# Performance work log

Measured on AMD Instinct MI355X. Metric: run time of the kernel, lower is better.

The kernel has to match this reference:

```python
import jax, jax.numpy as jnp
import numpy as np

ITER_STEPS = 2


def setup_inputs() -> dict:
    key = jax.random.key(0)
    ks = jax.random.split(key, 9)
    B, N, D, E = 64, 256, 512, 10  # batch, nodes, node_dim, edge types
    node = jax.random.normal(ks[0], (B, N, D), dtype=jnp.float32)
    node_mask = jax.random.randint(ks[1], (B, N), 0, 2).astype(jnp.int32)
    adj = jax.random.randint(ks[2], (E, B, N, N), 0, 2).astype(jnp.int32)
    s = 0.02
    W_nw = jax.random.normal(ks[3], (1, D), dtype=jnp.float32) * s   # node weight fc [out=1, in=D]
    b_nw = jnp.zeros((1,), dtype=jnp.float32)
    W_self = jax.random.normal(ks[4], (D, D), dtype=jnp.float32) * s
    b_self = jnp.zeros((D,), dtype=jnp.float32)
    W_edge = jax.random.normal(ks[5], (E, D, D), dtype=jnp.float32) * s  # per-edge-type Linear (no bias)
    return {"node": node, "W_nw": W_nw, "b_nw": b_nw, "W_self": W_self,
            "b_self": b_self, "W_edge": W_edge, "node_mask": node_mask, "adj": adj}


def reference(node, W_nw, b_nw, W_self, b_self, W_edge, node_mask, adj):
    # node: [B,N,D]; node_mask: [B,N] int; adj: [E=10,B,N,N] int (binary)
    B, N, D = node.shape
    m = node_mask.astype(node.dtype)
    eye = jnp.eye(N, dtype=node.dtype)
    # dd_graph = mask outer-product with zeroed diagonal: [B,N,N]
    dd = m[:, None, :] * m[:, :, None] * (1.0 - eye)
    graphs = dd[None] * adj.astype(node.dtype)  # [E,B,N,N]
    # total neighbor count across all 10 edge types, clamped to >=1 (replace_masked_values)
    neigh = graphs.sum(axis=(0, 3))                       # [B,N]
    neigh = jnp.where(neigh >= 1.0, neigh, 1.0)
    all_weight = []
    for _ in range(ITER_STEPS):
        # (1) node relatedness gate
        w = jax.nn.sigmoid(node @ W_nw.T + b_nw)[..., 0]  # [B,N]
        all_weight.append(w)
        self_info = node @ W_self.T + b_self              # [B,N,D]
        # (2) per-edge-type projection + masked adjacency matmul, summed over edge types
        proj = jnp.einsum('bnk,edk->ebnd', node, W_edge)  # [E,B,N,D]
        masked_w = jnp.where(graphs != 0, w[None, :, None, :], 0.0)  # [E,B,N,N]
        agg = jnp.einsum('ebnm,ebmd->bnd', masked_w, proj)           # [B,N,D]
        # (3) update
        node = jax.nn.relu(self_info + agg / neigh[..., None])
    return node, jnp.stack(all_weight, axis=1)  # ([B,N,D], [B,ITER,N])
```

## Files before the change

### kernel.cpp

```cpp
#include <hip/hip_runtime.h>
#include <hip/hip_bf16.h>

#define BB 64
#define NN 256
#define DD 512
#define EE 10

typedef __bf16 bf16x8 __attribute__((ext_vector_type(8)));
typedef unsigned short ushort8v __attribute__((ext_vector_type(8)));
typedef unsigned int uint4v __attribute__((ext_vector_type(4)));
typedef unsigned int uint2v __attribute__((ext_vector_type(2)));
typedef float floatx4 __attribute__((ext_vector_type(4)));
typedef float floatx16 __attribute__((ext_vector_type(16)));

typedef __attribute__((address_space(3))) unsigned short lds_us;
typedef const __attribute__((address_space(1))) unsigned short glb_us;

__device__ __forceinline__ unsigned short f2b(float f) {
    union { float f; unsigned u; } x; x.f = f;
    unsigned r = x.u + 0x7FFFu + ((x.u >> 16) & 1u);
    return (unsigned short)(r >> 16);
}
__device__ __forceinline__ float b2f(unsigned short u) {
    union { unsigned u; float f; } x; x.u = ((unsigned)u) << 16;
    return x.f;
}
__device__ __forceinline__ unsigned pack_bf16(float a, float b) {
    union { float f; unsigned u; } xa, xb2; xa.f = a; xb2.f = b;
    return __builtin_amdgcn_perm(xa.u + 0x8000u, xb2.u + 0x8000u, 0x07060302u);
}
__device__ __forceinline__ bf16x8 expand_byte(unsigned byte_) {
    uint4v av;
    #pragma unroll
    for (int p2 = 0; p2 < 4; p2++) {
        unsigned tt = (byte_ >> (2 * p2)) & 3u;
        av[p2] = ((tt | (tt << 15)) & 0x10001u) * 0x3F80u;
    }
    return __builtin_bit_cast(bf16x8, av);
}

__global__ void k_wconv(const float* __restrict__ W_edge,
                        const float* __restrict__ W_self,
                        unsigned short* __restrict__ Wf) {
    int t = blockIdx.x * 256 + threadIdx.x;
    int lane  = t & 63;
    int kstep = (t >> 6) & 31;
    int cfg   = (t >> 11) & 15;
    int e     = t >> 15;
    int dout = cfg * 32 + (lane & 31);
    int k    = kstep * 16 + (lane >> 5) * 8;
    const float* src = (e < EE) ? (W_edge + ((size_t)e * DD + dout) * DD + k)
                                : (W_self + (size_t)dout * DD + k);
    ushort8v o;
    #pragma unroll
    for (int j = 0; j < 8; j++) o[j] = f2b(src[j]);
    *(ushort8v*)(Wf + (size_t)t * 8) = o;
}

__global__ void k_graph(const int* __restrict__ adj, const int* __restrict__ mask,
                        unsigned* __restrict__ packed, float* __restrict__ recip) {
    int b = blockIdx.x >> 8;
    int n = blockIdx.x & 255;
    int lane = threadIdx.x & 63;
    int wv   = threadIdx.x >> 6;
    int m = wv * 64 + lane;
    int ok = (mask[b * NN + n] != 0) & (mask[b * NN + m] != 0) & (m != n);
    __shared__ int cnt_s[4];
    int total = 0;
    #pragma unroll
    for (int e = 0; e < EE; e++) {
        int a = adj[(((size_t)e * BB + b) * NN + n) * NN + m];
        int bit = ok & (a != 0);
        unsigned long long bal = __ballot(bit);
        if (lane == 0) {
            unsigned* dst = packed + (((size_t)e * BB + b) * NN + n) * 8 + wv * 2;
            dst[0] = (unsigned)bal;
            dst[1] = (unsigned)(bal >> 32);
        }
        total += bit;
    }
    for (int off = 32; off; off >>= 1) total += __shfl_down(total, off);
    if (lane == 0) cnt_s[wv] = total;
    __syncthreads();
    if (threadIdx.x == 0) {
        int c = cnt_s[0] + cnt_s[1] + cnt_s[2] + cnt_s[3];
        recip[b * NN + n] = 1.0f / (float)(c < 1 ? 1 : c);
    }
}

template<int TI>
__global__ __launch_bounds__(256)
void k_gt(const float* __restrict__ xf, const unsigned short* __restrict__ xbin,
          const float* __restrict__ W_nw, const float* __restrict__ b_nw,
          float* __restrict__ w_out, unsigned short* __restrict__ wTf,
          unsigned short* __restrict__ xb0) {
    int bid = blockIdx.x;
    int b  = bid >> 4;
    int ms = bid & 15;
    __shared__ float part[16][17];
    __shared__ float wsig[16];
    int t = threadIdx.x;
    int row = t >> 4;
    int seg = t & 15;
    size_t g = ((size_t)(b * NN + ms * 16 + row)) * DD + seg * 32;
    float s = 0.f;
    if (TI == 0) {
        const floatx4* xp = (const floatx4*)(xf + g);
        const floatx4* wp = (const floatx4*)(W_nw + seg * 32);
        #pragma unroll
        for (int k = 0; k < 4; k++) {
            floatx4 a = xp[2 * k], c4 = xp[2 * k + 1];
            floatx4 wa = wp[2 * k], wc = wp[2 * k + 1];
            ushort8v u;
            #pragma unroll
            for (int j = 0; j < 4; j++) {
                s += a[j] * wa[j] + c4[j] * wc[j];
                u[j] = f2b(a[j]); u[4 + j] = f2b(c4[j]);
            }
            *(ushort8v*)(xb0 + g + k * 8) = u;
        }
    } else {
        const ushort8v* xp = (const ushort8v*)(xbin + g);
        const float* wp = W_nw + seg * 32;
        #pragma unroll
        for (int k = 0; k < 4; k++) {
            ushort8v u = xp[k];
            #pragma unroll
            for (int j = 0; j < 8; j++) s += b2f(u[j]) * wp[k * 8 + j];
        }
    }
    part[row][seg] = s;
    __syncthreads();
    if (t < 16) {
        float tot = 0.f;
        #pragma unroll
        for (int i = 0; i < 16; i++) tot += part[t][i];
        float v = 1.f / (1.f + __expf(-(tot + b_nw[0])));
        wsig[t] = v;
        w_out[(b * 2 + TI) * NN + ms * 16 + t] = v;
    }
    __syncthreads();
    #pragma unroll
    for (int c = 0; c < 4; c++) {
        int slot = t + 256 * c;
        int dd_  = slot >> 6;
        int lane = slot & 63;
        int l31 = lane & 31, hi = lane >> 5;
        size_t xrow = ((size_t)(b * NN + ms * 16 + hi * 8)) * DD + dd_ * 32 + l31;
        ushort8v o;
        #pragma unroll
        for (int j = 0; j < 8; j++) {
            float xv = (TI == 0) ? xf[xrow + (size_t)j * DD] : b2f(xbin[xrow + (size_t)j * DD]);
            o[j] = f2b(xv * wsig[hi * 8 + j]);
        }
        *(ushort8v*)(wTf + ((((size_t)b * 16 + ms) * 16 + dd_) * 64 + lane) * 8) = o;
    }
}

template<int TI>
__global__ __launch_bounds__(512, 4)
void k2_heavy(const unsigned short* __restrict__ wTf,
              const unsigned short* __restrict__ xb,
              const unsigned short* __restrict__ Wf,
              const unsigned* __restrict__ packed,
              const float* __restrict__ recip,
              const float* __restrict__ b_self,
              unsigned short* __restrict__ out_bf16,
              float* __restrict__ out_f32) {
    __shared__ __attribute__((aligned(16))) unsigned short sWT[64 * 512];
    __shared__ __attribute__((aligned(16))) unsigned short sTf[16 * 512];

    int bid = blockIdx.x;
    int ct = bid & 1;
    int b  = (bid >> 1) & 63;
    int nq = bid >> 7;
    int w = threadIdx.x >> 6, lane = threadIdx.x & 63;
    int l31 = lane & 31, hi = lane >> 5;

    int s1_d = w >> 1, s1_nb = w & 1;
    int gn1 = nq * 64 + s1_nb * 32 + l31;
    float rn = recip[b * NN + gn1];

    floatx16 acc2[2];
    #pragma unroll
    for (int i = 0; i < 2; i++)
        #pragma unroll
        for (int q = 0; q < 16; q++) acc2[i][q] = 0.f;

    auto stage_sWT = [&](int dc2) {
        #pragma unroll
        for (int it = 0; it < 8; it++) {
            int c = it * 8 + w;
            const unsigned short* g = wTf +
                ((((size_t)b * 16 + (c >> 2)) * 16 + dc2 * 4 + (c & 3)) * 64 + lane) * 8;
            __builtin_amdgcn_global_load_lds((glb_us*)g, (lds_us*)&sWT[c * 512], 16, 0, 0);
        }
    };

    stage_sWT(0);

    const unsigned short* WfL = Wf + lane * 8;
    const unsigned short* xbL = xb + ((size_t)(b * NN + nq * 64 + l31)) * DD + hi * 8;

    unsigned pw[8];

    #pragma unroll 1
    for (int s = 0; s < 40; s++) {
        int e = s >> 2, dc2 = s & 3;
        asm volatile("s_waitcnt vmcnt(0) lgkmcnt(0)" ::: "memory");
        __builtin_amdgcn_s_barrier();
        if ((s & 3) == 0) {
            const uint4v* pp = (const uint4v*)(packed +
                (((size_t)e * BB + b) * NN + gn1) * 8);
            uint4v pa = pp[0], pbv = pp[1];
            pw[0] = pa[0]; pw[1] = pa[1]; pw[2] = pa[2]; pw[3] = pa[3];
            pw[4] = pbv[0]; pw[5] = pbv[1]; pw[6] = pbv[2]; pw[7] = pbv[3];
        }
        {
            floatx16 acc3a, acc3b;
            #pragma unroll
            for (int q = 0; q < 16; q++) { acc3a[q] = 0.f; acc3b[q] = 0.f; }
            #pragma unroll
            for (int ks = 0; ks < 8; ks++) {
                bf16x8 afrA = __builtin_bit_cast(bf16x8,
                    *(const ushort8v*)&sWT[((2 * ks) * 4 + s1_d) * 512 + lane * 8]);
                bf16x8 afrB = __builtin_bit_cast(bf16x8,
                    *(const ushort8v*)&sWT[((2 * ks + 1) * 4 + s1_d) * 512 + lane * 8]);
                unsigned wrd = pw[ks];
                bf16x8 bgA = expand_byte((wrd >> (hi * 8)) & 0xFFu);
                bf16x8 bgB = expand_byte((wrd >> ((2 + hi) * 8)) & 0xFFu);
                acc3a = __builtin_amdgcn_mfma_f32_32x32x16_bf16(afrA, bgA, acc3a, 0, 0, 0);
                acc3b = __builtin_amdgcn_mfma_f32_32x32x16_bf16(afrB, bgB, acc3b, 0, 0, 0);
            }
            #pragma unroll
            for (int g = 0; g < 4; g++) {
                float v0 = (acc3a[g * 4 + 0] + acc3b[g * 4 + 0]) * rn;
                float v1 = (acc3a[g * 4 + 1] + acc3b[g * 4 + 1]) * rn;
                float v2 = (acc3a[g * 4 + 2] + acc3b[g * 4 + 2]) * rn;
                float v3 = (acc3a[g * 4 + 3] + acc3b[g * 4 + 3]) * rn;
                uint2v pk;
                pk[0] = pack_bf16(v1, v0);
                pk[1] = pack_bf16(v3, v2);
                int kk_w = s1_d * 2 + (g >> 1);
                int slot = (kk_w * 2 + s1_nb) * 64 + (g & 1) * 32 + l31;
                *(uint2v*)&sTf[slot * 8 + 4 * hi] = pk;
            }
        }
        asm volatile("s_waitcnt lgkmcnt(0)" ::: "memory");
        __builtin_amdgcn_s_barrier();
        if (s + 1 < 40) stage_sWT((s + 1) & 3);
        #pragma unroll
        for (int kk = 0; kk < 8; kk++) {
            bf16x8 bfr = __builtin_bit_cast(bf16x8, *(const ushort8v*)
                &WfL[(size_t)(((e * 16 + ct * 8 + w) * 32 + dc2 * 8 + kk)) * 512]);
            bf16x8 afr0 = __builtin_bit_cast(bf16x8,
                *(const ushort8v*)&sTf[((kk * 2 + 0) * 64 + lane) * 8]);
            bf16x8 afr1 = __builtin_bit_cast(bf16x8,
                *(const ushort8v*)&sTf[((kk * 2 + 1) * 64 + lane) * 8]);
            acc2[0] = __builtin_amdgcn_mfma_f32_32x32x16_bf16(afr0, bfr, acc2[0], 0, 0, 0);
            acc2[1] = __builtin_amdgcn_mfma_f32_32x32x16_bf16(afr1, bfr, acc2[1], 0, 0, 0);
        }
    }
    #pragma unroll 1
    for (int dc2 = 0; dc2 < 4; dc2++) {
        #pragma unroll
        for (int kk = 0; kk < 8; kk++) {
            bf16x8 bfr = __builtin_bit_cast(bf16x8, *(const ushort8v*)
                &WfL[(size_t)(((EE * 16 + ct * 8 + w) * 32 + dc2 * 8 + kk)) * 512]);
            bf16x8 afr0 = __builtin_bit_cast(bf16x8, *(const ushort8v*)
                &xbL[(size_t)0 * 32 * DD + (dc2 * 8 + kk) * 16]);
            bf16x8 afr1 = __builtin_bit_cast(bf16x8, *(const ushort8v*)
                &xbL[(size_t)1 * 32 * DD + (dc2 * 8 + kk) * 16]);
            acc2[0] = __builtin_amdgcn_mfma_f32_32x32x16_bf16(afr0, bfr, acc2[0], 0, 0, 0);
            acc2[1] = __builtin_amdgcn_mfma_f32_32x32x16_bf16(afr1, bfr, acc2[1], 0, 0, 0);
        }
    }
    {
        int col = ct * 256 + w * 32 + l31;
        float bs = b_self[col];
        #pragma unroll
        for (int nb = 0; nb < 2; nb++) {
            #pragma unroll
            for (int rg = 0; rg < 16; rg++) {
                int row = nq * 64 + nb * 32 + (rg & 3) + 8 * (rg >> 2) + 4 * hi;
                float v = acc2[nb][rg] + bs;
                v = v > 0.f ? v : 0.f;
                size_t gi = ((size_t)b * NN + row) * DD + col;
                if (TI == 0) out_bf16[gi] = f2b(v);
                else         out_f32[gi] = v;
            }
        }
    }
}

extern "C" void kernel_launch(void* const* d_in, const int* in_sizes, int n_in,
                              void* d_out, int out_size, void* d_ws, size_t ws_size,
                              hipStream_t stream) {
    const float* node   = (const float*)d_in[0];
    const float* W_nw   = (const float*)d_in[1];
    const float* b_nw   = (const float*)d_in[2];
    const float* W_self = (const float*)d_in[3];
    const float* b_self = (const float*)d_in[4];
    const float* W_edge = (const float*)d_in[5];
    const int*   mask   = (const int*)d_in[6];
    const int*   adj    = (const int*)d_in[7];
    float* out = (float*)d_out;
    float* out_w = out + (size_t)BB * NN * DD;

    char* ws = (char*)d_ws;
    size_t off = 0;
    unsigned short* Wf    = (unsigned short*)(ws + off); off += (size_t)11 * DD * DD * 2;
    unsigned short* wTf   = (unsigned short*)(ws + off); off += (size_t)BB * DD * NN * 2;
    unsigned short* xb0   = (unsigned short*)(ws + off); off += (size_t)BB * NN * DD * 2;
    unsigned short* xb1   = (unsigned short*)(ws + off); off += (size_t)BB * NN * DD * 2;
    unsigned*       packed= (unsigned*)(ws + off);       off += (size_t)EE * BB * NN * 8 * 4;
    float*          recip = (float*)(ws + off);          off += (size_t)BB * NN * 4;

    k_wconv<<<dim3(1408), dim3(256), 0, stream>>>(W_edge, W_self, Wf);
    k_graph<<<dim3(16384), dim3(256), 0, stream>>>(adj, mask, packed, recip);

    k_gt<0><<<dim3(1024), dim3(256), 0, stream>>>(node, nullptr, W_nw, b_nw, out_w, wTf, xb0);
    k2_heavy<0><<<dim3(512), dim3(512), 0, stream>>>(wTf, xb0, Wf, packed, recip, b_self, xb1, nullptr);

    k_gt<1><<<dim3(1024), dim3(256), 0, stream>>>(nullptr, xb1, W_nw, b_nw, out_w, wTf, nullptr);
    k2_heavy<1><<<dim3(512), dim3(512), 0, stream>>>(wTf, xb1, Wf, packed, recip, b_self, nullptr, out);
}
```

Measured before the change: 769.9 us.

## Hoist mask expansion per edge type, merge stage-1 accumulators, defer neighbor scaling

The adjacency bit-to-bf16 expansion is precomputed once per edge type into 32 registers of spread nibbles, then turned into MFMA fragments each step with cheap byte-permute operations. The two stage-1 accumulators are merged into one 16-step MFMA chain. The 1/neigh scaling moves from each stage-1 output to a single per-row multiply on the final edge accumulator before the self-projection is added. This removes repeated bit expansion and per-step multiplies, at the cost of more register pressure, a serial MFMA dependency chain, and bf16 rounding of unscaled intermediate values.

```diff
diff --git a/kernel.cpp b/kernel.cpp
--- a/kernel.cpp
+++ b/kernel.cpp
@@ -29,13 +29,14 @@
     union { float f; unsigned u; } xa, xb2; xa.f = a; xb2.f = b;
     return __builtin_amdgcn_perm(xa.u + 0x8000u, xb2.u + 0x8000u, 0x07060302u);
 }
-__device__ __forceinline__ bf16x8 expand_byte(unsigned byte_) {
+__device__ __forceinline__ bf16x8 frag_from_nibs(unsigned n0, unsigned n1) {
+    unsigned r80a = n0 << 7, r80b = n1 << 7;
+    unsigned r3fa = n0 * 63u, r3fb = n1 * 63u;
     uint4v av;
-    #pragma unroll
-    for (int p2 = 0; p2 < 4; p2++) {
-        unsigned tt = (byte_ >> (2 * p2)) & 3u;
-        av[p2] = ((tt | (tt << 15)) & 0x10001u) * 0x3F80u;
-    }
+    av[0] = __builtin_amdgcn_perm(r3fa, r80a, 0x05010400u);
+    av[1] = __builtin_amdgcn_perm(r3fa, r80a, 0x07030602u);
+    av[2] = __builtin_amdgcn_perm(r3fb, r80b, 0x05010400u);
+    av[3] = __builtin_amdgcn_perm(r3fb, r80b, 0x07030602u);
     return __builtin_bit_cast(bf16x8, av);
 }
 
@@ -179,7 +180,6 @@
 
     int s1_d = w >> 1, s1_nb = w & 1;
     int gn1 = nq * 64 + s1_nb * 32 + l31;
-    float rn = recip[b * NN + gn1];
 
     floatx16 acc2[2];
     #pragma unroll
@@ -202,7 +202,7 @@
     const unsigned short* WfL = Wf + lane * 8;
     const unsigned short* xbL = xb + ((size_t)(b * NN + nq * 64 + l31)) * DD + hi * 8;
 
-    unsigned pw[8];
+    unsigned bq[32];
 
     #pragma unroll 1
     for (int s = 0; s < 40; s++) {
@@ -213,34 +213,34 @@
             const uint4v* pp = (const uint4v*)(packed +
                 (((size_t)e * BB + b) * NN + gn1) * 8);
             uint4v pa = pp[0], pbv = pp[1];
-            pw[0] = pa[0]; pw[1] = pa[1]; pw[2] = pa[2]; pw[3] = pa[3];
-            pw[4] = pbv[0]; pw[5] = pbv[1]; pw[6] = pbv[2]; pw[7] = pbv[3];
+            unsigned pwv[8] = {pa[0], pa[1], pa[2], pa[3], pbv[0], pbv[1], pbv[2], pbv[3]};
+            #pragma unroll
+            for (int ks = 0; ks < 8; ks++) {
+                unsigned byA = (pwv[ks] >> (hi * 8)) & 0xFFu;
+                unsigned byB = (pwv[ks] >> ((2 + hi) * 8)) & 0xFFu;
+                bq[ks * 4 + 0] = ((byA & 0xFu) * 0x00204081u) & 0x01010101u;
+                bq[ks * 4 + 1] = (((byA >> 4) & 0xFu) * 0x00204081u) & 0x01010101u;
+                bq[ks * 4 + 2] = ((byB & 0xFu) * 0x00204081u) & 0x01010101u;
+                bq[ks * 4 + 3] = (((byB >> 4) & 0xFu) * 0x00204081u) & 0x01010101u;
+            }
         }
         {
-            floatx16 acc3a, acc3b;
-            #pragma unroll
-            for (int q = 0; q < 16; q++) { acc3a[q] = 0.f; acc3b[q] = 0.f; }
-            #pragma unroll
-            for (int ks = 0; ks < 8; ks++) {
-                bf16x8 afrA = __builtin_bit_cast(bf16x8,
-                    *(const ushort8v*)&sWT[((2 * ks) * 4 + s1_d) * 512 + lane * 8]);
-                bf16x8 afrB = __builtin_bit_cast(bf16x8,
-                    *(const ushort8v*)&sWT[((2 * ks + 1) * 4 + s1_d) * 512 + lane * 8]);
-                unsigned wrd = pw[ks];
-                bf16x8 bgA = expand_byte((wrd >> (hi * 8)) & 0xFFu);
-                bf16x8 bgB = expand_byte((wrd >> ((2 + hi) * 8)) & 0xFFu);
-                acc3a = __builtin_amdgcn_mfma_f32_32x32x16_bf16(afrA, bgA, acc3a, 0, 0, 0);
-                acc3b = __builtin_amdgcn_mfma_f32_32x32x16_bf16(afrB, bgB, acc3b, 0, 0, 0);
+            floatx16 acc3;
+            #pragma unroll
+            for (int q = 0; q < 16; q++) acc3[q] = 0.f;
+            #pragma unroll
+            for (int mk = 0; mk < 16; mk++) {
+                bf16x8 afr = __builtin_bit_cast(bf16x8,
+                    *(const ushort8v*)&sWT[(mk * 4 + s1_d) * 512 + lane * 8]);
+                bf16x8 bg = frag_from_nibs(bq[(mk >> 1) * 4 + (mk & 1) * 2],
+                                           bq[(mk >> 1) * 4 + (mk & 1) * 2 + 1]);
+                acc3 = __builtin_amdgcn_mfma_f32_32x32x16_bf16(afr, bg, acc3, 0, 0, 0);
             }
             #pragma unroll
             for (int g = 0; g < 4; g++) {
-                float v0 = (acc3a[g * 4 + 0] + acc3b[g * 4 + 0]) * rn;
-                float v1 = (acc3a[g * 4 + 1] + acc3b[g * 4 + 1]) * rn;
-                float v2 = (acc3a[g * 4 + 2] + acc3b[g * 4 + 2]) * rn;
-                float v3 = (acc3a[g * 4 + 3] + acc3b[g * 4 + 3]) * rn;
                 uint2v pk;
-                pk[0] = pack_bf16(v1, v0);
-                pk[1] = pack_bf16(v3, v2);
+                pk[0] = pack_bf16(acc3[g * 4 + 1], acc3[g * 4 + 0]);
+                pk[1] = pack_bf16(acc3[g * 4 + 3], acc3[g * 4 + 2]);
                 int kk_w = s1_d * 2 + (g >> 1);
                 int slot = (kk_w * 2 + s1_nb) * 64 + (g & 1) * 32 + l31;
                 *(uint2v*)&sTf[slot * 8 + 4 * hi] = pk;
@@ -259,6 +259,14 @@
                 *(const ushort8v*)&sTf[((kk * 2 + 1) * 64 + lane) * 8]);
             acc2[0] = __builtin_amdgcn_mfma_f32_32x32x16_bf16(afr0, bfr, acc2[0], 0, 0, 0);
             acc2[1] = __builtin_amdgcn_mfma_f32_32x32x16_bf16(afr1, bfr, acc2[1], 0, 0, 0);
+        }
+    }
+    #pragma unroll
+    for (int nb = 0; nb < 2; nb++) {
+        #pragma unroll
+        for (int rg = 0; rg < 16; rg++) {
+            int row = nq * 64 + nb * 32 + (rg & 3) + 8 * (rg >> 2) + 4 * hi;
+            acc2[nb][rg] *= recip[b * NN + row];
         }
     }
     #pragma unroll 1
```

New measurement: 721.6 us. 1.07x faster.
